# Kernel optimization log

Measured on AMD Instinct MI355X. Metric: run time of the kernel, lower is better.

Reference implementation:

```python
import jax, jax.numpy as jnp
import numpy as np

K = 8
LOCAL_WINDOW_RATIO = 0.25
NEG = -1e9
LN_EPS = 1e-5
NORM_EPS = 1e-12


def _window_indices(H, W):
    lws = max(3, int(min(H, W) * LOCAL_WINDOW_RATIO))
    if lws % 2 == 0:
        lws += 1
    half = lws // 2
    off = jnp.arange(-half, half + 1)
    dy, dx = jnp.meshgrid(off, off, indexing='ij')          # [lws,lws]
    dy = dy.reshape(-1); dx = dx.reshape(-1)                 # [w2]
    py, px = jnp.meshgrid(jnp.arange(H), jnp.arange(W), indexing='ij')
    py = py.reshape(-1); px = px.reshape(-1)                 # [HW]
    ny = py[:, None] + dy[None, :]                           # [HW,w2]
    nx = px[:, None] + dx[None, :]
    valid = (ny >= 0) & (ny < H) & (nx >= 0) & (nx < W)
    idx = jnp.clip(ny, 0, H - 1) * W + jnp.clip(nx, 0, W - 1)
    return idx, valid


def setup_inputs() -> dict:
    key = jax.random.key(0)
    ks = jax.random.split(key, 5)
    B, C, H, W = 4, 96, 48, 48
    return {
        'x': jax.random.normal(ks[0], (B, C, H, W), jnp.float32),
        'w1': jax.random.normal(ks[1], (2 * C, C), jnp.float32) * 0.05,
        'b1': jax.random.normal(ks[2], (2 * C,), jnp.float32) * 0.05,
        'w2': jax.random.normal(ks[3], (C, 2 * C), jnp.float32) * 0.05,
        'b2': jax.random.normal(ks[4], (C,), jnp.float32) * 0.05,
        'ln_w': jnp.ones((C,), jnp.float32),
        'ln_b': jnp.zeros((C,), jnp.float32),
    }


def reference(x, w1, b1, w2, b2, ln_w, ln_b):
    B, C, H, W = x.shape
    HW = H * W
    idx_w, valid = _window_indices(H, W)                     # [HW,w2]

    x_flat = x.transpose(0, 2, 3, 1).reshape(B, HW, C)       # [B,HW,C]
    n = jnp.linalg.norm(x_flat, axis=-1, keepdims=True)
    x_n = x_flat / jnp.maximum(n, NORM_EPS)

    win_n = x_n[:, idx_w, :]                                 # [B,HW,w2,C]
    sims = jnp.einsum('bpc,bpwc->bpw', x_n, win_n)           # cosine sim
    sims = jnp.where(valid[None], sims, NEG)

    # every pixel has >= (half+1)^2 >= K valid neighbors, so top-k stays valid
    top_sim, top_idx = jax.lax.top_k(sims, K)                # [B,HW,K]
    wts = jax.nn.softmax(top_sim, axis=-1)                   # exp/sum over top-k

    idx_g = jnp.take_along_axis(jnp.broadcast_to(idx_w[None], sims.shape), top_idx, axis=-1)  # [B,HW,K]
    feats = x_flat[jnp.arange(B)[:, None, None], idx_g]      # [B,HW,K,C] (un-normalized)
    agg = jnp.einsum('bpk,bpkc->bpc', wts, feats)            # [B,HW,C]

    mu = jnp.mean(x_flat, axis=-1, keepdims=True)
    var = jnp.var(x_flat, axis=-1, keepdims=True)
    x_ln = (x_flat - mu) / jnp.sqrt(var + LN_EPS) * ln_w + ln_b

    enhanced = agg + x_ln                                    # [B,HW,C]
    h = jax.nn.relu(jnp.einsum('bpc,dc->bpd', enhanced, w1) + b1)
    ffn = jnp.einsum('bpd,cd->bpc', h, w2) + b2
    out = enhanced + ffn
    return out.reshape(B, H, W, C).transpose(0, 3, 1, 2)
```

## Files before the change

### kernel.cpp

```cpp
#include <hip/hip_runtime.h>
#include <math.h>

#define BATCH 4
#define CH    96
#define HH    48
#define WW    48
#define HWPIX (HH*WW)
#define NPIX  (BATCH*HWPIX)
#define WIN   13
#define WIN2  169
#define HALF  6
#define TOPK  8
#define NEGV  (-1000000000.0f)

__global__ __launch_bounds__(256) void k0_wt(
    const float* __restrict__ w1, const float* __restrict__ w2,
    float* __restrict__ w1T, float* __restrict__ w2T)
{
    __shared__ float tile[32][33];
    int bid = blockIdx.x;
    const float* src; float* dst; int R, C, tr, tc;
    if (bid < 18) { src = w1; dst = w1T; R = 192; C = 96;  tr = bid / 3; tc = bid % 3; }
    else { int b2 = bid - 18; src = w2; dst = w2T; R = 96; C = 192; tr = b2 / 6; tc = b2 % 6; }
    int r0 = tr * 32, c0 = tc * 32;
    int tx = threadIdx.x & 31, ty = threadIdx.x >> 5;

    #pragma unroll
    for (int i = 0; i < 4; ++i) {
        int r = ty + i * 8;
        tile[r][tx] = src[(r0 + r) * C + c0 + tx];
    }
    __syncthreads();
    #pragma unroll
    for (int i = 0; i < 4; ++i) {
        int r = ty + i * 8;
        dst[(c0 + r) * R + r0 + tx] = tile[tx][r];
    }
}

__global__ __launch_bounds__(256) void k1_prep(
    const float* __restrict__ x, float* __restrict__ xt2,
    float* __restrict__ invn, float* __restrict__ muv, float* __restrict__ rsd)
{
    __shared__ float lds[96][33];
    int bid = blockIdx.x;
    int b   = bid / 72;
    int p0  = (bid % 72) * 32;
    int t   = threadIdx.x;

    #pragma unroll
    for (int it = 0; it < 12; ++it) {
        int e = t + it * 256;
        int c = e >> 5;
        int p = e & 31;
        lds[c][p] = x[(b * CH + c) * HWPIX + p0 + p];
    }
    __syncthreads();

    if (t < 32) {
        float s = 0.f, ss = 0.f;
        #pragma unroll
        for (int c = 0; c < CH; ++c) { float v = lds[c][t]; s += v; ss += v * v; }
        int gpix = b * HWPIX + p0 + t;
        invn[gpix] = 1.0f / fmaxf(sqrtf(ss), 1e-12f);
        float m = s * (1.0f / 96.0f);
        muv[gpix] = m;
        rsd[gpix] = rsqrtf(ss * (1.0f / 96.0f) - m * m + 1e-5f);
    }

    float4* x4 = (float4*)xt2;
    #pragma unroll
    for (int it = 0; it < 3; ++it) {
        int i = t + it * 256;
        int p = i & 31;
        int s = i >> 5;
        float4 v = make_float4(lds[4*s][p], lds[4*s+1][p],
                               lds[4*s+2][p], lds[4*s+3][p]);
        x4[s * NPIX + b * HWPIX + p0 + p] = v;
    }
}

__global__ __launch_bounds__(256) void k2_knn(
    const float* __restrict__ xt2, const float* __restrict__ invn,
    const float* __restrict__ muv, const float* __restrict__ rsd,
    const float* __restrict__ lnw, const float* __restrict__ lnb,
    float* __restrict__ enh)
{
    __shared__ float own[4][96];
    int t    = threadIdx.x;
    int wv   = t >> 6;
    int lane = t & 63;
    int gp   = blockIdx.x * 4 + wv;
    int b    = gp / HWPIX;
    int p    = gp - b * HWPIX;
    int py   = p / WW;
    int px   = p - py * WW;
    const float4* x4 = (const float4*)xt2;

    float4 ownv = make_float4(0.f, 0.f, 0.f, 0.f);
    if (lane < 24) {
        ownv = x4[lane * NPIX + gp];
        ((float4*)(own[wv]))[lane] = ownv;
    }
    float inp = invn[gp];
    float mu  = muv[gp];
    float rs  = rsd[gp];

    float v0 = -2e9f, v1 = -2e9f, v2 = -2e9f;
    const float4* ov = (const float4*)(own[wv]);
    #pragma unroll
    for (int k = 0; k < 3; ++k) {
        int n = lane + 64 * k;
        float sim = -2e9f;
        if (n < WIN2) {
            int dy = n / WIN - HALF;
            int dx = n - (dy + HALF) * WIN - HALF;
            int ny = py + dy, nx = px + dx;
            if (ny >= 0 && ny < HH && nx >= 0 && nx < WW) {
                int q = b * HWPIX + ny * WW + nx;
                float inq = invn[q];
                const float4* rp = x4 + q;
                float ax = 0.f, ay = 0.f, az = 0.f, aw = 0.f;
                #pragma unroll
                for (int s = 0; s < 24; ++s) {
                    float4 a  = ov[s];
                    float4 bb = rp[s * NPIX];
                    ax += a.x * bb.x; ay += a.y * bb.y;
                    az += a.z * bb.z; aw += a.w * bb.w;
                }
                sim = ((ax + ay) + (az + aw)) * inp * inq;
            } else {
                sim = NEGV;
            }
        }
        if (k == 0) v0 = sim; else if (k == 1) v1 = sim; else v2 = sim;
    }

    float tv[TOPK]; int tn[TOPK];
    #pragma unroll
    for (int r = 0; r < TOPK; ++r) {
        float m = fmaxf(fmaxf(v0, v1), v2);
        #pragma unroll
        for (int off = 1; off < 64; off <<= 1)
            m = fmaxf(m, __shfl_xor(m, off));
        unsigned long long m0 = __ballot(v0 == m);
        unsigned long long m1 = __ballot(v1 == m);
        unsigned long long m2 = __ballot(v2 == m);
        int n;
        if (m0)      n = (int)__builtin_ctzll(m0);
        else if (m1) n = 64 + (int)__builtin_ctzll(m1);
        else         n = 128 + (int)__builtin_ctzll(m2);
        tv[r] = m; tn[r] = n;
        int kk = n >> 6, ll = n & 63;
        if (ll == lane) {
            if (kk == 0)      v0 = -2e9f;
            else if (kk == 1) v1 = -2e9f;
            else              v2 = -2e9f;
        }
    }

    float wts[TOPK]; int qn[TOPK];
    float wsum = 0.f;
    #pragma unroll
    for (int r = 0; r < TOPK; ++r) {
        float e = expf(tv[r] - tv[0]);
        wts[r] = e; wsum += e;
        int n  = tn[r];
        int dy = n / WIN - HALF;
        int dx = n - (dy + HALF) * WIN - HALF;
        int gy = min(max(py + dy, 0), HH - 1);
        int gx = min(max(px + dx, 0), WW - 1);
        qn[r]  = b * HWPIX + gy * WW + gx;
    }
    float winv = 1.0f / wsum;

    if (lane < 24) {
        const float4* base = x4 + lane * NPIX;
        float4 g = make_float4(0.f, 0.f, 0.f, 0.f);
        #pragma unroll
        for (int r = 0; r < TOPK; ++r) {
            float4 f = base[qn[r]];
            float w = wts[r];
            g.x += w * f.x; g.y += w * f.y;
            g.z += w * f.z; g.w += w * f.w;
        }
        float4 lw = ((const float4*)lnw)[lane];
        float4 lb = ((const float4*)lnb)[lane];
        float4 e;
        e.x = g.x * winv + (ownv.x - mu) * rs * lw.x + lb.x;
        e.y = g.y * winv + (ownv.y - mu) * rs * lw.y + lb.y;
        e.z = g.z * winv + (ownv.z - mu) * rs * lw.z + lb.z;
        e.w = g.w * winv + (ownv.w - mu) * rs * lw.w + lb.w;
        ((float4*)(enh + gp * CH))[lane] = e;
    }
}

__global__ __launch_bounds__(192) void k3_ffn(
    const float* __restrict__ enh, const float* __restrict__ w1T,
    const float* __restrict__ b1, const float* __restrict__ w2T,
    const float* __restrict__ b2, float* __restrict__ out)
{
    __shared__ float hl[4][200];
    int g  = blockIdx.x;
    int b  = g / 576;
    int p0 = (g % 576) * 4;
    int t  = threadIdx.x;

    {
        int j = t;
        const float4* e0 = (const float4*)(enh + (b * HWPIX + p0 + 0) * CH);
        const float4* e1 = (const float4*)(enh + (b * HWPIX + p0 + 1) * CH);
        const float4* e2 = (const float4*)(enh + (b * HWPIX + p0 + 2) * CH);
        const float4* e3 = (const float4*)(enh + (b * HWPIX + p0 + 3) * CH);
        float a0 = 0.f, a1 = 0.f, a2 = 0.f, a3 = 0.f;
        #pragma unroll 6
        for (int c4 = 0; c4 < 24; ++c4) {
            float wa = w1T[(4*c4 + 0) * 192 + j];
            float wb = w1T[(4*c4 + 1) * 192 + j];
            float wc = w1T[(4*c4 + 2) * 192 + j];
            float wd = w1T[(4*c4 + 3) * 192 + j];
            float4 v0 = e0[c4];
            float4 v1 = e1[c4];
            float4 v2 = e2[c4];
            float4 v3 = e3[c4];
            a0 += v0.x*wa + v0.y*wb + v0.z*wc + v0.w*wd;
            a1 += v1.x*wa + v1.y*wb + v1.z*wc + v1.w*wd;
            a2 += v2.x*wa + v2.y*wb + v2.z*wc + v2.w*wd;
            a3 += v3.x*wa + v3.y*wb + v3.z*wc + v3.w*wd;
        }
        float bj = b1[j];
        hl[0][j] = fmaxf(a0 + bj, 0.f);
        hl[1][j] = fmaxf(a1 + bj, 0.f);
        hl[2][j] = fmaxf(a2 + bj, 0.f);
        hl[3][j] = fmaxf(a3 + bj, 0.f);
    }
    __syncthreads();

    if (t < 96) {
        int c = t;
        const float4* h0 = (const float4*)(&hl[0][0]);
        const float4* h1 = (const float4*)(&hl[1][0]);
        const float4* h2 = (const float4*)(&hl[2][0]);
        const float4* h3 = (const float4*)(&hl[3][0]);
        float s0 = 0.f, s1 = 0.f, s2 = 0.f, s3 = 0.f;
        #pragma unroll 6
        for (int j4 = 0; j4 < 48; ++j4) {
            float wa = w2T[(4*j4 + 0) * 96 + c];
            float wb = w2T[(4*j4 + 1) * 96 + c];
            float wc = w2T[(4*j4 + 2) * 96 + c];
            float wd = w2T[(4*j4 + 3) * 96 + c];
            float4 u0 = h0[j4], u1 = h1[j4], u2 = h2[j4], u3 = h3[j4];
            s0 += u0.x*wa + u0.y*wb + u0.z*wc + u0.w*wd;
            s1 += u1.x*wa + u1.y*wb + u1.z*wc + u1.w*wd;
            s2 += u2.x*wa + u2.y*wb + u2.z*wc + u2.w*wd;
            s3 += u3.x*wa + u3.y*wb + u3.z*wc + u3.w*wd;
        }
        float bc = b2[c];
        out[(b * CH + c) * HWPIX + p0 + 0] =
            enh[(b * HWPIX + p0 + 0) * CH + c] + s0 + bc;
        out[(b * CH + c) * HWPIX + p0 + 1] =
            enh[(b * HWPIX + p0 + 1) * CH + c] + s1 + bc;
        out[(b * CH + c) * HWPIX + p0 + 2] =
            enh[(b * HWPIX + p0 + 2) * CH + c] + s2 + bc;
        out[(b * CH + c) * HWPIX + p0 + 3] =
            enh[(b * HWPIX + p0 + 3) * CH + c] + s3 + bc;
    }
}

extern "C" void kernel_launch(void* const* d_in, const int* in_sizes, int n_in,
                              void* d_out, int out_size, void* d_ws, size_t ws_size,
                              hipStream_t stream)
{
    const float* x   = (const float*)d_in[0];
    const float* w1  = (const float*)d_in[1];
    const float* b1  = (const float*)d_in[2];
    const float* w2  = (const float*)d_in[3];
    const float* b2  = (const float*)d_in[4];
    const float* lnw = (const float*)d_in[5];
    const float* lnb = (const float*)d_in[6];
    float* out = (float*)d_out;

    float* xt2 = out;

    float* ws   = (float*)d_ws;
    float* enh  = ws;
    float* invn = enh + NPIX * CH;
    float* muv  = invn + NPIX;
    float* rsd  = muv + NPIX;
    float* w1T  = rsd + NPIX;
    float* w2T  = w1T + 192 * 96;

    hipLaunchKernelGGL(k0_wt, dim3(36), dim3(256), 0, stream,
                       w1, w2, w1T, w2T);
    hipLaunchKernelGGL(k1_prep, dim3(288), dim3(256), 0, stream,
                       x, xt2, invn, muv, rsd);
    hipLaunchKernelGGL(k2_knn, dim3(NPIX / 4), dim3(256), 0, stream,
                       xt2, invn, muv, rsd, lnw, lnb, enh);
    hipLaunchKernelGGL(k3_ffn, dim3(2304), dim3(192), 0, stream,
                       enh, w1T, b1, w2T, b2, out);
}
```

Measured before the change: 76.35 us.

## Fuse KNN aggregation with FFN kernel and halve prep tile size

The KNN/LayerNorm kernel and the FFN kernel are merged so each block keeps its four enhanced pixel vectors in shared memory and runs both FFN matmuls plus the residual directly. This removes the global write and re-read of the enhanced tensor and one kernel launch. The output is written as a float4 over four consecutive pixels. The transposed input buffer now lives in workspace rather than aliasing the output. The prep kernel now uses 16-pixel tiles across twice as many blocks. The fused block carries more shared memory and registers, which may reduce occupancy, and shared-memory loads become scalar instead of float4.

```diff
diff --git a/kernel.cpp b/kernel.cpp
--- a/kernel.cpp
+++ b/kernel.cpp
@@ -42,22 +42,22 @@
     const float* __restrict__ x, float* __restrict__ xt2,
     float* __restrict__ invn, float* __restrict__ muv, float* __restrict__ rsd)
 {
-    __shared__ float lds[96][33];
+    __shared__ float lds[96][17];
     int bid = blockIdx.x;
-    int b   = bid / 72;
-    int p0  = (bid % 72) * 32;
+    int b   = bid / 144;
+    int p0  = (bid % 144) * 16;
     int t   = threadIdx.x;
 
     #pragma unroll
-    for (int it = 0; it < 12; ++it) {
+    for (int it = 0; it < 6; ++it) {
         int e = t + it * 256;
-        int c = e >> 5;
-        int p = e & 31;
+        int c = e >> 4;
+        int p = e & 15;
         lds[c][p] = x[(b * CH + c) * HWPIX + p0 + p];
     }
     __syncthreads();
 
-    if (t < 32) {
+    if (t < 16) {
         float s = 0.f, ss = 0.f;
         #pragma unroll
         for (int c = 0; c < CH; ++c) { float v = lds[c][t]; s += v; ss += v * v; }
@@ -69,24 +69,26 @@
     }
 
     float4* x4 = (float4*)xt2;
-    #pragma unroll
-    for (int it = 0; it < 3; ++it) {
-        int i = t + it * 256;
-        int p = i & 31;
-        int s = i >> 5;
+    for (int i = t; i < 384; i += 256) {
+        int p = i & 15;
+        int s = i >> 4;
         float4 v = make_float4(lds[4*s][p], lds[4*s+1][p],
                                lds[4*s+2][p], lds[4*s+3][p]);
         x4[s * NPIX + b * HWPIX + p0 + p] = v;
     }
 }
 
-__global__ __launch_bounds__(256) void k2_knn(
+__global__ __launch_bounds__(256) void k2_fused(
     const float* __restrict__ xt2, const float* __restrict__ invn,
     const float* __restrict__ muv, const float* __restrict__ rsd,
     const float* __restrict__ lnw, const float* __restrict__ lnb,
-    float* __restrict__ enh)
+    const float* __restrict__ w1T, const float* __restrict__ b1,
+    const float* __restrict__ w2T, const float* __restrict__ b2,
+    float* __restrict__ out)
 {
     __shared__ float own[4][96];
+    __shared__ float enh_l[4][100];
+    __shared__ float hl[4][200];
     int t    = threadIdx.x;
     int wv   = t >> 6;
     int lane = t & 63;
@@ -186,32 +188,16 @@
         }
         float4 lw = ((const float4*)lnw)[lane];
         float4 lb = ((const float4*)lnb)[lane];
-        float4 e;
-        e.x = g.x * winv + (ownv.x - mu) * rs * lw.x + lb.x;
-        e.y = g.y * winv + (ownv.y - mu) * rs * lw.y + lb.y;
-        e.z = g.z * winv + (ownv.z - mu) * rs * lw.z + lb.z;
-        e.w = g.w * winv + (ownv.w - mu) * rs * lw.w + lb.w;
-        ((float4*)(enh + gp * CH))[lane] = e;
-    }
-}
-
-__global__ __launch_bounds__(192) void k3_ffn(
-    const float* __restrict__ enh, const float* __restrict__ w1T,
-    const float* __restrict__ b1, const float* __restrict__ w2T,
-    const float* __restrict__ b2, float* __restrict__ out)
-{
-    __shared__ float hl[4][200];
-    int g  = blockIdx.x;
-    int b  = g / 576;
-    int p0 = (g % 576) * 4;
-    int t  = threadIdx.x;
-
-    {
+        int c0 = lane * 4;
+        enh_l[wv][c0 + 0] = g.x * winv + (ownv.x - mu) * rs * lw.x + lb.x;
+        enh_l[wv][c0 + 1] = g.y * winv + (ownv.y - mu) * rs * lw.y + lb.y;
+        enh_l[wv][c0 + 2] = g.z * winv + (ownv.z - mu) * rs * lw.z + lb.z;
+        enh_l[wv][c0 + 3] = g.w * winv + (ownv.w - mu) * rs * lw.w + lb.w;
+    }
+    __syncthreads();
+
+    if (t < 192) {
         int j = t;
-        const float4* e0 = (const float4*)(enh + (b * HWPIX + p0 + 0) * CH);
-        const float4* e1 = (const float4*)(enh + (b * HWPIX + p0 + 1) * CH);
-        const float4* e2 = (const float4*)(enh + (b * HWPIX + p0 + 2) * CH);
-        const float4* e3 = (const float4*)(enh + (b * HWPIX + p0 + 3) * CH);
         float a0 = 0.f, a1 = 0.f, a2 = 0.f, a3 = 0.f;
         #pragma unroll 6
         for (int c4 = 0; c4 < 24; ++c4) {
@@ -219,14 +205,15 @@
             float wb = w1T[(4*c4 + 1) * 192 + j];
             float wc = w1T[(4*c4 + 2) * 192 + j];
             float wd = w1T[(4*c4 + 3) * 192 + j];
-            float4 v0 = e0[c4];
-            float4 v1 = e1[c4];
-            float4 v2 = e2[c4];
-            float4 v3 = e3[c4];
-            a0 += v0.x*wa + v0.y*wb + v0.z*wc + v0.w*wd;
-            a1 += v1.x*wa + v1.y*wb + v1.z*wc + v1.w*wd;
-            a2 += v2.x*wa + v2.y*wb + v2.z*wc + v2.w*wd;
-            a3 += v3.x*wa + v3.y*wb + v3.z*wc + v3.w*wd;
+            int cc = 4 * c4;
+            float e0a = enh_l[0][cc], e0b = enh_l[0][cc+1], e0c = enh_l[0][cc+2], e0d = enh_l[0][cc+3];
+            float e1a = enh_l[1][cc], e1b = enh_l[1][cc+1], e1c = enh_l[1][cc+2], e1d = enh_l[1][cc+3];
+            float e2a = enh_l[2][cc], e2b = enh_l[2][cc+1], e2c = enh_l[2][cc+2], e2d = enh_l[2][cc+3];
+            float e3a = enh_l[3][cc], e3b = enh_l[3][cc+1], e3c = enh_l[3][cc+2], e3d = enh_l[3][cc+3];
+            a0 += e0a*wa + e0b*wb + e0c*wc + e0d*wd;
+            a1 += e1a*wa + e1b*wb + e1c*wc + e1d*wd;
+            a2 += e2a*wa + e2b*wb + e2c*wc + e2d*wd;
+            a3 += e3a*wa + e3b*wb + e3c*wc + e3d*wd;
         }
         float bj = b1[j];
         hl[0][j] = fmaxf(a0 + bj, 0.f);
@@ -238,10 +225,6 @@
 
     if (t < 96) {
         int c = t;
-        const float4* h0 = (const float4*)(&hl[0][0]);
-        const float4* h1 = (const float4*)(&hl[1][0]);
-        const float4* h2 = (const float4*)(&hl[2][0]);
-        const float4* h3 = (const float4*)(&hl[3][0]);
         float s0 = 0.f, s1 = 0.f, s2 = 0.f, s3 = 0.f;
         #pragma unroll 6
         for (int j4 = 0; j4 < 48; ++j4) {
@@ -249,21 +232,26 @@
             float wb = w2T[(4*j4 + 1) * 96 + c];
             float wc = w2T[(4*j4 + 2) * 96 + c];
             float wd = w2T[(4*j4 + 3) * 96 + c];
-            float4 u0 = h0[j4], u1 = h1[j4], u2 = h2[j4], u3 = h3[j4];
-            s0 += u0.x*wa + u0.y*wb + u0.z*wc + u0.w*wd;
-            s1 += u1.x*wa + u1.y*wb + u1.z*wc + u1.w*wd;
-            s2 += u2.x*wa + u2.y*wb + u2.z*wc + u2.w*wd;
-            s3 += u3.x*wa + u3.y*wb + u3.z*wc + u3.w*wd;
+            int jj = 4 * j4;
+            float h0a = hl[0][jj], h0b = hl[0][jj+1], h0c = hl[0][jj+2], h0d = hl[0][jj+3];
+            float h1a = hl[1][jj], h1b = hl[1][jj+1], h1c = hl[1][jj+2], h1d = hl[1][jj+3];
+            float h2a = hl[2][jj], h2b = hl[2][jj+1], h2c = hl[2][jj+2], h2d = hl[2][jj+3];
+            float h3a = hl[3][jj], h3b = hl[3][jj+1], h3c = hl[3][jj+2], h3d = hl[3][jj+3];
+            s0 += h0a*wa + h0b*wb + h0c*wc + h0d*wd;
+            s1 += h1a*wa + h1b*wb + h1c*wc + h1d*wd;
+            s2 += h2a*wa + h2b*wb + h2c*wc + h2d*wd;
+            s3 += h3a*wa + h3b*wb + h3c*wc + h3d*wd;
         }
         float bc = b2[c];
-        out[(b * CH + c) * HWPIX + p0 + 0] =
-            enh[(b * HWPIX + p0 + 0) * CH + c] + s0 + bc;
-        out[(b * CH + c) * HWPIX + p0 + 1] =
-            enh[(b * HWPIX + p0 + 1) * CH + c] + s1 + bc;
-        out[(b * CH + c) * HWPIX + p0 + 2] =
-            enh[(b * HWPIX + p0 + 2) * CH + c] + s2 + bc;
-        out[(b * CH + c) * HWPIX + p0 + 3] =
-            enh[(b * HWPIX + p0 + 3) * CH + c] + s3 + bc;
+        int gp0 = blockIdx.x * 4;
+        int bb  = gp0 / HWPIX;
+        int pp0 = gp0 - bb * HWPIX;
+        float4 o;
+        o.x = enh_l[0][c] + s0 + bc;
+        o.y = enh_l[1][c] + s1 + bc;
+        o.z = enh_l[2][c] + s2 + bc;
+        o.w = enh_l[3][c] + s3 + bc;
+        *(float4*)(out + (bb * CH + c) * HWPIX + pp0) = o;
     }
 }
 
@@ -280,11 +268,9 @@
     const float* lnb = (const float*)d_in[6];
     float* out = (float*)d_out;
 
-    float* xt2 = out;
-
     float* ws   = (float*)d_ws;
-    float* enh  = ws;
-    float* invn = enh + NPIX * CH;
+    float* xt2  = ws;
+    float* invn = xt2 + NPIX * CH;
     float* muv  = invn + NPIX;
     float* rsd  = muv + NPIX;
     float* w1T  = rsd + NPIX;
@@ -292,10 +278,8 @@
 
     hipLaunchKernelGGL(k0_wt, dim3(36), dim3(256), 0, stream,
                        w1, w2, w1T, w2T);
-    hipLaunchKernelGGL(k1_prep, dim3(288), dim3(256), 0, stream,
+    hipLaunchKernelGGL(k1_prep, dim3(576), dim3(256), 0, stream,
                        x, xt2, invn, muv, rsd);
-    hipLaunchKernelGGL(k2_knn, dim3(NPIX / 4), dim3(256), 0, stream,
-                       xt2, invn, muv, rsd, lnw, lnb, enh);
-    hipLaunchKernelGGL(k3_ffn, dim3(2304), dim3(192), 0, stream,
-                       enh, w1T, b1, w2T, b2, out);
-}
+    hipLaunchKernelGGL(k2_fused, dim3(NPIX / 4), dim3(256), 0, stream,
+                       xt2, invn, muv, rsd, lnw, lnb, w1T, b1, w2T, b2, out);
+}
```

New measurement: 85.61 us. +12.1%, slower.
